# Kernel optimization log

Hardware: AMD Instinct MI355X
Metric: run time of the kernel (lower is better)

## Reference

```python
import jax, jax.numpy as jnp
import numpy as np

EMBED_DIM = 1024
NUM_HEADS = 16
HEAD_DIM = EMBED_DIM // NUM_HEADS


def setup_inputs() -> dict:
    key = jax.random.key(0)
    ks = jax.random.split(key, 9)
    B, S, E = 4, 2048, EMBED_DIM
    # xavier_uniform bound for square [E, E] weights
    bound = float(np.sqrt(6.0 / (E + E)))
    def w(k):
        return jax.random.uniform(k, (E, E), jnp.float32, -bound, bound)
    return {
        "x": jax.random.normal(ks[0], (B, S, E), jnp.float32),
        "Wq": w(ks[1]), "bq": jnp.zeros((E,), jnp.float32),
        "Wk": w(ks[2]), "bk": jnp.zeros((E,), jnp.float32),
        "Wv": w(ks[3]), "bv": jnp.zeros((E,), jnp.float32),
        "Wo": w(ks[4]), "bo": jnp.zeros((E,), jnp.float32),
    }


def reference(x, Wq, bq, Wk, bk, Wv, bv, Wo, bo):
    B, S, E = x.shape
    H, D = NUM_HEADS, HEAD_DIM
    # Linear projections (torch Linear: x @ W.T + b)
    q = (x @ Wq.T + bq).reshape(B, S, H, D)
    k = (x @ Wk.T + bk).reshape(B, S, H, D)
    v = (x @ Wv.T + bv).reshape(B, S, H, D)
    # per-head scaled dot-product attention (vectorized over heads)
    scores = jnp.einsum("bqhd,bkhd->bhqk", q, k) / jnp.sqrt(jnp.float32(D))
    attn = jax.nn.softmax(scores, axis=-1)
    o = jnp.einsum("bhqk,bkhd->bqhd", attn, v).reshape(B, S, E)
    return o @ Wo.T + bo
```

## Files before the change

kernel.cpp:

```cpp
#include <hip/hip_runtime.h>
#include <stdint.h>

typedef unsigned short u16;
typedef short bf16x8 __attribute__((ext_vector_type(8)));
typedef float f32x4 __attribute__((ext_vector_type(4)));
typedef float f32x16 __attribute__((ext_vector_type(16)));

#define B_ 4
#define S_ 2048
#define H_ 16
#define D_ 64
#define E_ 1024
#define M_ (B_ * S_)

static __device__ __forceinline__ u16 f2bf(float f) {
  uint32_t u = __builtin_bit_cast(uint32_t, f);
  u += 0x7fffu + ((u >> 16) & 1u);
  return (u16)(u >> 16);
}
static __device__ __forceinline__ uint32_t pack2bf(float a, float b) {
  return (uint32_t)f2bf(a) | ((uint32_t)f2bf(b) << 16);
}
static __device__ __forceinline__ uint32_t cvt_pk_bf16(float a, float b) {
  uint32_t r;
  asm("v_cvt_pk_bf16_f32 %0, %1, %2" : "=v"(r) : "v"(a), "v"(b));
  return r;
}
static __device__ __forceinline__ void pl32swap(uint32_t& a, uint32_t& b) {
  asm volatile("v_permlane32_swap_b32 %0, %1" : "+v"(a), "+v"(b));
}

static __device__ __forceinline__ void gld_lds16(const void* g, void* l) {
  __builtin_amdgcn_global_load_lds(
      (const __attribute__((address_space(1))) void*)(uintptr_t)g,
      (__attribute__((address_space(3))) void*)(uint32_t)(uintptr_t)l, 16, 0, 0);
}

__global__ __launch_bounds__(256) void cvt_f32_bf16(const float* __restrict__ in,
                                                    u16* __restrict__ out, int n) {
  int i = (blockIdx.x * 256 + threadIdx.x) * 8;
  if (i + 8 > n) return;
  float4 a = *(const float4*)(in + i);
  float4 b = *(const float4*)(in + i + 4);
  struct __align__(16) U8 { u16 h[8]; } u;
  u.h[0] = f2bf(a.x); u.h[1] = f2bf(a.y); u.h[2] = f2bf(a.z); u.h[3] = f2bf(a.w);
  u.h[4] = f2bf(b.x); u.h[5] = f2bf(b.y); u.h[6] = f2bf(b.z); u.h[7] = f2bf(b.w);
  *(U8*)(out + i) = u;
}

__global__ __launch_bounds__(256) void cvt_w4(const float* __restrict__ w0,
                                              const float* __restrict__ w1,
                                              const float* __restrict__ w2,
                                              const float* __restrict__ w3,
                                              u16* __restrict__ out) {
  const int NW_BLK = (E_ * E_) / 2048;
  const int seg = blockIdx.x >> 9;
  const float* src = seg == 0 ? w0 : seg == 1 ? w1 : seg == 2 ? w2 : w3;
  int i = ((blockIdx.x & (NW_BLK - 1)) * 256 + threadIdx.x) * 8;
  float4 a = *(const float4*)(src + i);
  float4 b = *(const float4*)(src + i + 4);
  struct __align__(16) U8 { u16 h[8]; } u;
  u.h[0] = f2bf(a.x); u.h[1] = f2bf(a.y); u.h[2] = f2bf(a.z); u.h[3] = f2bf(a.w);
  u.h[4] = f2bf(b.x); u.h[5] = f2bf(b.y); u.h[6] = f2bf(b.z); u.h[7] = f2bf(b.w);
  *(U8*)(out + (size_t)seg * (E_ * E_) + i) = u;
}

template <int KIND, typename OutT>
static __device__ __forceinline__ void gemm128(const u16* __restrict__ A,
                                               const u16* __restrict__ W,
                                               const float* __restrict__ bias,
                                               OutT* __restrict__ C, int m0, int n0,
                                               float scale, u16* As, u16* Bs) {
  const int tid = threadIdx.x;
  const int wave = tid >> 6, lane = tid & 63;
  const int col16 = lane & 15, quad = lane >> 4;
  const int wm = wave >> 1, wn = wave & 1;

  f32x4 acc[4][4] = {};

  const int r0 = tid >> 3;
  const int sg8 = ((tid & 7) ^ (r0 & 7)) * 8;
  const u16* ga = A + (size_t)(m0 + r0) * E_ + sg8;
  const u16* gb = W + (size_t)(n0 + r0) * E_ + sg8;
  u16* lA = As + wave * 512;
  u16* lB = Bs + wave * 512;

  auto stage = [&](int k0, int buf) {
#pragma unroll
    for (int i = 0; i < 4; i++) {
      gld_lds16(ga + (size_t)(i * 32) * E_ + k0, lA + buf * 8192 + i * 2048);
      gld_lds16(gb + (size_t)(i * 32) * E_ + k0, lB + buf * 8192 + i * 2048);
    }
  };

  stage(0, 0);
  const int NK = E_ / 64;
  for (int kk = 0; kk < NK; kk++) {
    asm volatile("s_waitcnt vmcnt(0)" ::: "memory");
    __builtin_amdgcn_s_barrier();
    if (kk + 1 < NK) stage((kk + 1) * 64, (kk + 1) & 1);

    const u16* AsC = As + (kk & 1) * 8192;
    const u16* BsC = Bs + (kk & 1) * 8192;

    bf16x8 af[4][2], bw[4][2];
#pragma unroll
    for (int mt = 0; mt < 4; mt++)
#pragma unroll
      for (int ks = 0; ks < 2; ks++)
        af[mt][ks] = *(const bf16x8*)&AsC[(wm * 64 + mt * 16 + col16) * 64 +
                                          (((ks * 4 + quad) ^ (col16 & 7)) * 8)];
#pragma unroll
    for (int nt = 0; nt < 4; nt++)
#pragma unroll
      for (int ks = 0; ks < 2; ks++)
        bw[nt][ks] = *(const bf16x8*)&BsC[(wn * 64 + nt * 16 + col16) * 64 +
                                          (((ks * 4 + quad) ^ (col16 & 7)) * 8)];
#pragma unroll
    for (int ks = 0; ks < 2; ks++)
#pragma unroll
      for (int a = 0; a < 4; a++)
#pragma unroll
        for (int b = 0; b < 4; b++) {
          if constexpr (KIND == 2)
            acc[a][b] = __builtin_amdgcn_mfma_f32_16x16x32_bf16(af[a][ks], bw[b][ks], acc[a][b], 0, 0, 0);
          else
            acc[a][b] = __builtin_amdgcn_mfma_f32_16x16x32_bf16(bw[a][ks], af[b][ks], acc[a][b], 0, 0, 0);
        }
  }

  if constexpr (KIND == 2) {
#pragma unroll
    for (int a = 0; a < 4; a++) {
      int t = m0 + wm * 64 + a * 16 + quad * 4;
      int bb = t >> 11, s = t & (S_ - 1);
#pragma unroll
      for (int b = 0; b < 4; b++) {
        int oc = n0 + wn * 64 + b * 16 + col16;
        int h = oc >> 6, d = oc & 63;
        float bv = bias[oc];
        uint32_t lo = pack2bf(acc[a][b][0] + bv, acc[a][b][1] + bv);
        uint32_t hi = pack2bf(acc[a][b][2] + bv, acc[a][b][3] + bv);
        uint2 pk = {lo, hi};
        *(uint2*)&C[(((size_t)(bb * H_ + h) * D_ + d) * S_) + s] = pk;
      }
    }
  } else {
#pragma unroll
    for (int b = 0; b < 4; b++) {
      int row = m0 + wm * 64 + b * 16 + col16;
#pragma unroll
      for (int a = 0; a < 4; a++) {
        int nc = n0 + wn * 64 + a * 16 + quad * 4;
        float4 bv = *(const float4*)&bias[nc];
        float v0 = (acc[a][b][0] + bv.x) * scale;
        float v1 = (acc[a][b][1] + bv.y) * scale;
        float v2 = (acc[a][b][2] + bv.z) * scale;
        float v3 = (acc[a][b][3] + bv.w) * scale;
        if constexpr (KIND == 0) {
          uint2 pk = {pack2bf(v0, v1), pack2bf(v2, v3)};
          *(uint2*)&((u16*)C)[(size_t)row * E_ + nc] = pk;
        } else {
          float4 pk = {v0, v1, v2, v3};
          *(float4*)&((float*)C)[(size_t)row * E_ + nc] = pk;
        }
      }
    }
  }
}

__global__ __launch_bounds__(256) void gemm_qkv(const u16* __restrict__ xb,
                                                const u16* __restrict__ wq, const u16* __restrict__ wk,
                                                const u16* __restrict__ wv,
                                                const float* __restrict__ bq, const float* __restrict__ bk,
                                                const float* __restrict__ bv,
                                                u16* __restrict__ Qb, u16* __restrict__ Kb,
                                                u16* __restrict__ Vtb) {
  __shared__ __align__(16) u16 As[2][128 * 64];
  __shared__ __align__(16) u16 Bs[2][128 * 64];
  const int mat = blockIdx.x >> 3;
  const int n0 = (blockIdx.x & 7) * 128;
  const int m0 = blockIdx.y * 128;
  if (mat == 0)
    gemm128<0, u16>(xb, wq, bq, Qb, m0, n0, 0.125f * 1.44269504f, &As[0][0], &Bs[0][0]);
  else if (mat == 1)
    gemm128<0, u16>(xb, wk, bk, Kb, m0, n0, 1.0f, &As[0][0], &Bs[0][0]);
  else
    gemm128<2, u16>(xb, wv, bv, Vtb, m0, n0, 1.0f, &As[0][0], &Bs[0][0]);
}

__global__ __launch_bounds__(256) void gemm_out(const u16* __restrict__ Ob,
                                                const u16* __restrict__ wob,
                                                const float* __restrict__ bo,
                                                float* __restrict__ out) {
  __shared__ __align__(16) u16 As[2][128 * 64];
  __shared__ __align__(16) u16 Bs[2][128 * 64];
  gemm128<1, float>(Ob, wob, bo, out, blockIdx.y * 128, blockIdx.x * 128, 1.0f,
                    &As[0][0], &Bs[0][0]);
}

__global__ __launch_bounds__(512) void flash_attn(const u16* __restrict__ Q,
                                                  const u16* __restrict__ K,
                                                  const u16* __restrict__ Vt,
                                                  u16* __restrict__ O) {
  __shared__ __align__(16) u16 Ks[2][2][64 * 64];
  __shared__ __align__(16) u16 Vs[2][2][64 * 64];
  const int bid = blockIdx.x;
  const int qt = bid & 7, h = (bid >> 3) & 15, b = bid >> 7;
  const int tid = threadIdx.x;
  const int wave = tid >> 6, lane = tid & 63;
  const int l31 = lane & 31, hi = lane >> 5;
  const int sw7 = l31 & 7;

  const int srow = tid >> 3;
  const int sgrp = (tid & 7) ^ (srow & 7);
  const u16* Kbase = K + ((size_t)(b * S_) * H_ + h) * D_;
  const u16* Vbase = Vt + ((size_t)(b * H_ + h) * D_) * S_;

  auto stage = [&](int r, int buf) {
#pragma unroll
    for (int sub = 0; sub < 2; sub++) {
      gld_lds16(Kbase + (size_t)(r * 128 + sub * 64 + srow) * (H_ * D_) + sgrp * 8,
                &Ks[buf][sub][wave * 512]);
      gld_lds16(Vbase + (size_t)srow * S_ + r * 128 + sub * 64 + sgrp * 8,
                &Vs[buf][sub][wave * 512]);
    }
  };

  stage(0, 0);

  const int qrow = qt * 256 + wave * 32;
  bf16x8 qf[4];
  const u16* qp = Q + ((size_t)(b * S_ + qrow + l31) * H_ + h) * D_ + hi * 8;
#pragma unroll
  for (int t = 0; t < 4; t++) qf[t] = *(const bf16x8*)(qp + t * 16);

  f32x16 o_acc[2] = {};
  float l_sum = 0.f;

  const int NR = S_ / 128;
  for (int r = 0; r < NR; r++) {
    asm volatile("s_waitcnt vmcnt(0)" ::: "memory");
    __builtin_amdgcn_s_barrier();
    if (r + 1 < NR) stage(r + 1, (r + 1) & 1);
    const u16* KsC = &Ks[r & 1][0][0];
    const u16* VsC = &Vs[r & 1][0][0];

#pragma unroll
    for (int kblk = 0; kblk < 4; kblk++) {
      const u16* Ksub = KsC + (kblk >> 1) * 4096;
      const u16* Vsub = VsC + (kblk >> 1) * 4096;
      const int krow = (kblk & 1) * 32 + l31;
      f32x16 sacc = {};
      __builtin_amdgcn_s_setprio(1);
#pragma unroll
      for (int t = 0; t < 4; t++) {
        bf16x8 kf = *(const bf16x8*)&Ksub[krow * 64 + (((2 * t + hi) ^ sw7) * 8)];
        sacc = __builtin_amdgcn_mfma_f32_32x32x16_bf16(kf, qf[t], sacc, 0, 0, 0);
      }
      __builtin_amdgcn_s_setprio(0);

      float p[16];
#pragma unroll
      for (int e = 0; e < 16; e++) p[e] = __builtin_amdgcn_exp2f(sacc[e]);
      float s0 = (p[0] + p[1]) + (p[2] + p[3]);
      float s1 = (p[4] + p[5]) + (p[6] + p[7]);
      float s2 = (p[8] + p[9]) + (p[10] + p[11]);
      float s3 = (p[12] + p[13]) + (p[14] + p[15]);
      l_sum += (s0 + s1) + (s2 + s3);
      uint32_t W[8];
#pragma unroll
      for (int i = 0; i < 8; i++) W[i] = cvt_pk_bf16(p[2 * i], p[2 * i + 1]);

#pragma unroll
      for (int kf2 = 0; kf2 < 2; kf2++) {
        uint32_t w0 = W[kf2 * 4 + 0], w1 = W[kf2 * 4 + 1];
        uint32_t w2 = W[kf2 * 4 + 2], w3 = W[kf2 * 4 + 3];
        pl32swap(w0, w2);
        pl32swap(w1, w3);
        union { uint32_t w[4]; bf16x8 v; } u;
        u.w[0] = w0; u.w[1] = w1; u.w[2] = w2; u.w[3] = w3;
        const bf16x8 pa = u.v;
        const int kfs = (kblk & 1) * 2 + kf2;
        __builtin_amdgcn_s_setprio(1);
#pragma unroll
        for (int n = 0; n < 2; n++) {
          const int dr = n * 32 + l31;
          bf16x8 vf = *(const bf16x8*)&Vsub[dr * 64 + (((2 * kfs + hi) ^ sw7) * 8)];
          o_acc[n] = __builtin_amdgcn_mfma_f32_32x32x16_bf16(pa, vf, o_acc[n], 0, 0, 0);
        }
        __builtin_amdgcn_s_setprio(0);
      }
    }
  }

  float l_tot = l_sum + __shfl_xor(l_sum, 32);
  float inv = 1.f / l_tot;

#pragma unroll
  for (int r = 0; r < 16; r++) {
    const int ql = (r & 3) + 8 * (r >> 2) + 4 * hi;
    const float iq = __shfl(inv, ql);
    u16* op = O + ((size_t)(b * S_ + qrow + ql) * H_ + h) * D_ + l31;
#pragma unroll
    for (int n = 0; n < 2; n++) op[n * 32] = f2bf(o_acc[n][r] * iq);
  }
}

extern "C" void kernel_launch(void* const* d_in, const int* in_sizes, int n_in,
                              void* d_out, int out_size, void* d_ws, size_t ws_size,
                              hipStream_t stream) {
  (void)in_sizes; (void)n_in; (void)out_size; (void)ws_size;
  const float* x  = (const float*)d_in[0];
  const float* Wq = (const float*)d_in[1];
  const float* bq = (const float*)d_in[2];
  const float* Wk = (const float*)d_in[3];
  const float* bk = (const float*)d_in[4];
  const float* Wv = (const float*)d_in[5];
  const float* bv = (const float*)d_in[6];
  const float* Wo = (const float*)d_in[7];
  const float* bo = (const float*)d_in[8];
  float* out = (float*)d_out;

  const size_t NX = (size_t)M_ * E_;
  const size_t NW = (size_t)E_ * E_;
  u16* xb  = (u16*)d_ws;
  u16* wqb = xb + NX;
  u16* wkb = wqb + NW;
  u16* wvb = wkb + NW;
  u16* wob = wvb + NW;
  u16* Qb  = wob + NW;
  u16* Kb  = Qb + NX;
  u16* Vtb = Kb + NX;
  u16* Ob  = Vtb + NX;

  cvt_f32_bf16<<<NX / 2048, 256, 0, stream>>>(x, xb, (int)NX);
  cvt_w4<<<4 * (NW / 2048), 256, 0, stream>>>(Wq, Wk, Wv, Wo, wqb);

  gemm_qkv<<<dim3(24, 64), 256, 0, stream>>>(xb, wqb, wkb, wvb, bq, bk, bv, Qb, Kb, Vtb);
  flash_attn<<<B_ * H_ * (S_ / 256), 512, 0, stream>>>(Qb, Kb, Vtb, Ob);
  gemm_out<<<dim3(8, 64), 256, 0, stream>>>(Ob, wob, bo, out);
}
```

Measured before the change: 275.0 us.

## Process two query groups per wave in flash attention with 256-thread blocks

Each wave now handles 64 query rows as two 32-row groups, so every K and V fragment read from LDS feeds two MFMAs instead of one. Blocks shrink from 8 to 4 waves, and the staging loop issues twice as many loads per thread to fill the same K/V tiles. This halves LDS read traffic per MFMA. In exchange it doubles the accumulator and Q registers per wave and leaves fewer waves per block to hide latency, with launch bounds set to allow two blocks per CU.

```diff
diff --git a/kernel.cpp b/kernel.cpp
--- a/kernel.cpp
+++ b/kernel.cpp
@@ -199,10 +199,10 @@
                     &As[0][0], &Bs[0][0]);
 }
 
-__global__ __launch_bounds__(512) void flash_attn(const u16* __restrict__ Q,
-                                                  const u16* __restrict__ K,
-                                                  const u16* __restrict__ Vt,
-                                                  u16* __restrict__ O) {
+__global__ __launch_bounds__(256, 2) void flash_attn(const u16* __restrict__ Q,
+                                                     const u16* __restrict__ K,
+                                                     const u16* __restrict__ Vt,
+                                                     u16* __restrict__ O) {
   __shared__ __align__(16) u16 Ks[2][2][64 * 64];
   __shared__ __align__(16) u16 Vs[2][2][64 * 64];
   const int bid = blockIdx.x;
@@ -219,24 +219,29 @@
 
   auto stage = [&](int r, int buf) {
 #pragma unroll
-    for (int sub = 0; sub < 2; sub++) {
-      gld_lds16(Kbase + (size_t)(r * 128 + sub * 64 + srow) * (H_ * D_) + sgrp * 8,
-                &Ks[buf][sub][wave * 512]);
-      gld_lds16(Vbase + (size_t)srow * S_ + r * 128 + sub * 64 + sgrp * 8,
-                &Vs[buf][sub][wave * 512]);
-    }
+    for (int sub = 0; sub < 2; sub++)
+#pragma unroll
+      for (int half = 0; half < 2; half++) {
+        gld_lds16(Kbase + (size_t)(r * 128 + sub * 64 + half * 32 + srow) * (H_ * D_) + sgrp * 8,
+                  &Ks[buf][sub][half * 2048 + wave * 512]);
+        gld_lds16(Vbase + (size_t)(half * 32 + srow) * S_ + r * 128 + sub * 64 + sgrp * 8,
+                  &Vs[buf][sub][half * 2048 + wave * 512]);
+      }
   };
 
   stage(0, 0);
 
-  const int qrow = qt * 256 + wave * 32;
-  bf16x8 qf[4];
-  const u16* qp = Q + ((size_t)(b * S_ + qrow + l31) * H_ + h) * D_ + hi * 8;
-#pragma unroll
-  for (int t = 0; t < 4; t++) qf[t] = *(const bf16x8*)(qp + t * 16);
-
-  f32x16 o_acc[2] = {};
-  float l_sum = 0.f;
+  const int qrow = qt * 256 + wave * 64;
+  bf16x8 qf[2][4];
+#pragma unroll
+  for (int qg = 0; qg < 2; qg++) {
+    const u16* qp = Q + ((size_t)(b * S_ + qrow + qg * 32 + l31) * H_ + h) * D_ + hi * 8;
+#pragma unroll
+    for (int t = 0; t < 4; t++) qf[qg][t] = *(const bf16x8*)(qp + t * 16);
+  }
+
+  f32x16 o_acc[2][2] = {};
+  float l_sum[2] = {0.f, 0.f};
 
   const int NR = S_ / 128;
   for (int r = 0; r < NR; r++) {
@@ -251,59 +256,75 @@
       const u16* Ksub = KsC + (kblk >> 1) * 4096;
       const u16* Vsub = VsC + (kblk >> 1) * 4096;
       const int krow = (kblk & 1) * 32 + l31;
-      f32x16 sacc = {};
+      bf16x8 kf[4];
+#pragma unroll
+      for (int t = 0; t < 4; t++)
+        kf[t] = *(const bf16x8*)&Ksub[krow * 64 + (((2 * t + hi) ^ sw7) * 8)];
+      f32x16 sacc[2];
+      sacc[0] = (f32x16)0.f; sacc[1] = (f32x16)0.f;
       __builtin_amdgcn_s_setprio(1);
 #pragma unroll
       for (int t = 0; t < 4; t++) {
-        bf16x8 kf = *(const bf16x8*)&Ksub[krow * 64 + (((2 * t + hi) ^ sw7) * 8)];
-        sacc = __builtin_amdgcn_mfma_f32_32x32x16_bf16(kf, qf[t], sacc, 0, 0, 0);
+        sacc[0] = __builtin_amdgcn_mfma_f32_32x32x16_bf16(kf[t], qf[0][t], sacc[0], 0, 0, 0);
+        sacc[1] = __builtin_amdgcn_mfma_f32_32x32x16_bf16(kf[t], qf[1][t], sacc[1], 0, 0, 0);
       }
       __builtin_amdgcn_s_setprio(0);
 
-      float p[16];
-#pragma unroll
-      for (int e = 0; e < 16; e++) p[e] = __builtin_amdgcn_exp2f(sacc[e]);
-      float s0 = (p[0] + p[1]) + (p[2] + p[3]);
-      float s1 = (p[4] + p[5]) + (p[6] + p[7]);
-      float s2 = (p[8] + p[9]) + (p[10] + p[11]);
-      float s3 = (p[12] + p[13]) + (p[14] + p[15]);
-      l_sum += (s0 + s1) + (s2 + s3);
-      uint32_t W[8];
-#pragma unroll
-      for (int i = 0; i < 8; i++) W[i] = cvt_pk_bf16(p[2 * i], p[2 * i + 1]);
+      uint32_t W[2][8];
+#pragma unroll
+      for (int qg = 0; qg < 2; qg++) {
+        float p[16];
+#pragma unroll
+        for (int e = 0; e < 16; e++) p[e] = __builtin_amdgcn_exp2f(sacc[qg][e]);
+        float s0 = (p[0] + p[1]) + (p[2] + p[3]);
+        float s1 = (p[4] + p[5]) + (p[6] + p[7]);
+        float s2 = (p[8] + p[9]) + (p[10] + p[11]);
+        float s3 = (p[12] + p[13]) + (p[14] + p[15]);
+        l_sum[qg] += (s0 + s1) + (s2 + s3);
+#pragma unroll
+        for (int i = 0; i < 8; i++) W[qg][i] = cvt_pk_bf16(p[2 * i], p[2 * i + 1]);
+      }
 
 #pragma unroll
       for (int kf2 = 0; kf2 < 2; kf2++) {
-        uint32_t w0 = W[kf2 * 4 + 0], w1 = W[kf2 * 4 + 1];
-        uint32_t w2 = W[kf2 * 4 + 2], w3 = W[kf2 * 4 + 3];
-        pl32swap(w0, w2);
-        pl32swap(w1, w3);
-        union { uint32_t w[4]; bf16x8 v; } u;
-        u.w[0] = w0; u.w[1] = w1; u.w[2] = w2; u.w[3] = w3;
-        const bf16x8 pa = u.v;
+        bf16x8 pa[2];
+#pragma unroll
+        for (int qg = 0; qg < 2; qg++) {
+          uint32_t w0 = W[qg][kf2 * 4 + 0], w1 = W[qg][kf2 * 4 + 1];
+          uint32_t w2 = W[qg][kf2 * 4 + 2], w3 = W[qg][kf2 * 4 + 3];
+          pl32swap(w0, w2);
+          pl32swap(w1, w3);
+          union { uint32_t w[4]; bf16x8 v; } u;
+          u.w[0] = w0; u.w[1] = w1; u.w[2] = w2; u.w[3] = w3;
+          pa[qg] = u.v;
+        }
         const int kfs = (kblk & 1) * 2 + kf2;
         __builtin_amdgcn_s_setprio(1);
 #pragma unroll
         for (int n = 0; n < 2; n++) {
           const int dr = n * 32 + l31;
           bf16x8 vf = *(const bf16x8*)&Vsub[dr * 64 + (((2 * kfs + hi) ^ sw7) * 8)];
-          o_acc[n] = __builtin_amdgcn_mfma_f32_32x32x16_bf16(pa, vf, o_acc[n], 0, 0, 0);
+          o_acc[0][n] = __builtin_amdgcn_mfma_f32_32x32x16_bf16(pa[0], vf, o_acc[0][n], 0, 0, 0);
+          o_acc[1][n] = __builtin_amdgcn_mfma_f32_32x32x16_bf16(pa[1], vf, o_acc[1][n], 0, 0, 0);
         }
         __builtin_amdgcn_s_setprio(0);
       }
     }
   }
 
-  float l_tot = l_sum + __shfl_xor(l_sum, 32);
-  float inv = 1.f / l_tot;
-
-#pragma unroll
-  for (int r = 0; r < 16; r++) {
-    const int ql = (r & 3) + 8 * (r >> 2) + 4 * hi;
-    const float iq = __shfl(inv, ql);
-    u16* op = O + ((size_t)(b * S_ + qrow + ql) * H_ + h) * D_ + l31;
-#pragma unroll
-    for (int n = 0; n < 2; n++) op[n * 32] = f2bf(o_acc[n][r] * iq);
+#pragma unroll
+  for (int qg = 0; qg < 2; qg++) {
+    float l_tot = l_sum[qg] + __shfl_xor(l_sum[qg], 32);
+    float inv = 1.f / l_tot;
+
+#pragma unroll
+    for (int r = 0; r < 16; r++) {
+      const int ql = (r & 3) + 8 * (r >> 2) + 4 * hi;
+      const float iq = __shfl(inv, ql);
+      u16* op = O + ((size_t)(b * S_ + qrow + qg * 32 + ql) * H_ + h) * D_ + l31;
+#pragma unroll
+      for (int n = 0; n < 2; n++) op[n * 32] = f2bf(o_acc[qg][n][r] * iq);
+    }
   }
 }
 
@@ -338,6 +359,6 @@
   cvt_w4<<<4 * (NW / 2048), 256, 0, stream>>>(Wq, Wk, Wv, Wo, wqb);
 
   gemm_qkv<<<dim3(24, 64), 256, 0, stream>>>(xb, wqb, wkb, wvb, bq, bk, bv, Qb, Kb, Vtb);
-  flash_attn<<<B_ * H_ * (S_ / 256), 512, 0, stream>>>(Qb, Kb, Vtb, Ob);
+  flash_attn<<<B_ * H_ * (S_ / 256), 256, 0, stream>>>(Qb, Kb, Vtb, Ob);
   gemm_out<<<dim3(8, 64), 256, 0, stream>>>(Ob, wob, bo, out);
 }
```

Result: no change. 278.6 us (+1.3%).

## Pre-swizzle V into MFMA fragment order and load directly to registers

Applied to the files above, without the earlier changes.

The V projection epilogue now writes V in a per-head layout that matches the MFMA B-operand fragment order, so the attention kernel can load V fragments from global memory straight into registers. This removes V from shared memory. K staging moves to a triple-buffered 64-row ring with a prefetch distance of two, waited on with vmcnt(1), and launch bounds request 4 blocks per SM. The aim is to cut LDS traffic and capacity so occupancy can rise, at the cost of uncached-through-LDS global loads for V on every tile, more register pressure from holding eight V fragments, and more frequent barriers.

```diff
diff --git a/kernel.cpp b/kernel.cpp
--- a/kernel.cpp
+++ b/kernel.cpp
@@ -134,15 +134,20 @@
     for (int a = 0; a < 4; a++) {
       int t = m0 + wm * 64 + a * 16 + quad * 4;
       int bb = t >> 11, s = t & (S_ - 1);
+      int kb = s >> 6, w = s & 63;
+      int kfs = w >> 4, hi2 = (w >> 3) & 1, j0 = w & 7;
 #pragma unroll
       for (int b = 0; b < 4; b++) {
         int oc = n0 + wn * 64 + b * 16 + col16;
         int h = oc >> 6, d = oc & 63;
+        int nn = d >> 5, ld = d & 31;
         float bv = bias[oc];
         uint32_t lo = pack2bf(acc[a][b][0] + bv, acc[a][b][1] + bv);
         uint32_t hi = pack2bf(acc[a][b][2] + bv, acc[a][b][3] + bv);
         uint2 pk = {lo, hi};
-        *(uint2*)&C[(((size_t)(bb * H_ + h) * D_ + d) * S_) + s] = pk;
+        size_t off = (size_t)(bb * H_ + h) * (S_ * D_) + kb * 4096 +
+                     (nn * 4 + kfs) * 512 + ld * 16 + hi2 * 8 + j0;
+        *(uint2*)&C[off] = pk;
       }
     }
   } else {
@@ -175,7 +180,7 @@
                                                 const float* __restrict__ bq, const float* __restrict__ bk,
                                                 const float* __restrict__ bv,
                                                 u16* __restrict__ Qb, u16* __restrict__ Kb,
-                                                u16* __restrict__ Vtb) {
+                                                u16* __restrict__ V2b) {
   __shared__ __align__(16) u16 As[2][128 * 64];
   __shared__ __align__(16) u16 Bs[2][128 * 64];
   const int mat = blockIdx.x >> 3;
@@ -186,7 +191,7 @@
   else if (mat == 1)
     gemm128<0, u16>(xb, wk, bk, Kb, m0, n0, 1.0f, &As[0][0], &Bs[0][0]);
   else
-    gemm128<2, u16>(xb, wv, bv, Vtb, m0, n0, 1.0f, &As[0][0], &Bs[0][0]);
+    gemm128<2, u16>(xb, wv, bv, V2b, m0, n0, 1.0f, &As[0][0], &Bs[0][0]);
 }
 
 __global__ __launch_bounds__(256) void gemm_out(const u16* __restrict__ Ob,
@@ -199,12 +204,11 @@
                     &As[0][0], &Bs[0][0]);
 }
 
-__global__ __launch_bounds__(512) void flash_attn(const u16* __restrict__ Q,
-                                                  const u16* __restrict__ K,
-                                                  const u16* __restrict__ Vt,
-                                                  u16* __restrict__ O) {
-  __shared__ __align__(16) u16 Ks[2][2][64 * 64];
-  __shared__ __align__(16) u16 Vs[2][2][64 * 64];
+__global__ __launch_bounds__(512, 4) void flash_attn(const u16* __restrict__ Q,
+                                                     const u16* __restrict__ K,
+                                                     const u16* __restrict__ V2,
+                                                     u16* __restrict__ O) {
+  __shared__ __align__(16) u16 Ks[3][64 * 64];
   const int bid = blockIdx.x;
   const int qt = bid & 7, h = (bid >> 3) & 15, b = bid >> 7;
   const int tid = threadIdx.x;
@@ -215,19 +219,15 @@
   const int srow = tid >> 3;
   const int sgrp = (tid & 7) ^ (srow & 7);
   const u16* Kbase = K + ((size_t)(b * S_) * H_ + h) * D_;
-  const u16* Vbase = Vt + ((size_t)(b * H_ + h) * D_) * S_;
-
-  auto stage = [&](int r, int buf) {
-#pragma unroll
-    for (int sub = 0; sub < 2; sub++) {
-      gld_lds16(Kbase + (size_t)(r * 128 + sub * 64 + srow) * (H_ * D_) + sgrp * 8,
-                &Ks[buf][sub][wave * 512]);
-      gld_lds16(Vbase + (size_t)srow * S_ + r * 128 + sub * 64 + sgrp * 8,
-                &Vs[buf][sub][wave * 512]);
-    }
+  const u16* vp = V2 + (size_t)(b * H_ + h) * (S_ * D_) + l31 * 16 + hi * 8;
+
+  auto stageK = [&](int kb, int buf) {
+    gld_lds16(Kbase + (size_t)(kb * 64 + srow) * (H_ * D_) + sgrp * 8,
+              &Ks[buf][wave * 512]);
   };
 
-  stage(0, 0);
+  stageK(0, 0);
+  stageK(1, 1);
 
   const int qrow = qt * 256 + wave * 32;
   bf16x8 qf[4];
@@ -238,24 +238,33 @@
   f32x16 o_acc[2] = {};
   float l_sum = 0.f;
 
-  const int NR = S_ / 128;
-  for (int r = 0; r < NR; r++) {
-    asm volatile("s_waitcnt vmcnt(0)" ::: "memory");
+  const int NT = S_ / 64;
+  int cur = 0;
+  for (int kb = 0; kb < NT; kb++) {
+    asm volatile("s_waitcnt vmcnt(1)" ::: "memory");
     __builtin_amdgcn_s_barrier();
-    if (r + 1 < NR) stage(r + 1, (r + 1) & 1);
-    const u16* KsC = &Ks[r & 1][0][0];
-    const u16* VsC = &Vs[r & 1][0][0];
-
-#pragma unroll
-    for (int kblk = 0; kblk < 4; kblk++) {
-      const u16* Ksub = KsC + (kblk >> 1) * 4096;
-      const u16* Vsub = VsC + (kblk >> 1) * 4096;
-      const int krow = (kblk & 1) * 32 + l31;
+
+    bf16x8 vf[2][4];
+#pragma unroll
+    for (int n = 0; n < 2; n++)
+#pragma unroll
+      for (int kfs = 0; kfs < 4; kfs++)
+        vf[n][kfs] = *(const bf16x8*)(vp + (size_t)kb * 4096 + (n * 4 + kfs) * 512);
+
+    if (kb + 2 < NT) {
+      int nb = cur + 2; if (nb >= 3) nb -= 3;
+      stageK(kb + 2, nb);
+    }
+    const u16* KsC = Ks[cur];
+
+#pragma unroll
+    for (int kblk = 0; kblk < 2; kblk++) {
+      const int krow = kblk * 32 + l31;
       f32x16 sacc = {};
       __builtin_amdgcn_s_setprio(1);
 #pragma unroll
       for (int t = 0; t < 4; t++) {
-        bf16x8 kf = *(const bf16x8*)&Ksub[krow * 64 + (((2 * t + hi) ^ sw7) * 8)];
+        bf16x8 kf = *(const bf16x8*)&KsC[krow * 64 + (((2 * t + hi) ^ sw7) * 8)];
         sacc = __builtin_amdgcn_mfma_f32_32x32x16_bf16(kf, qf[t], sacc, 0, 0, 0);
       }
       __builtin_amdgcn_s_setprio(0);
@@ -281,17 +290,14 @@
         union { uint32_t w[4]; bf16x8 v; } u;
         u.w[0] = w0; u.w[1] = w1; u.w[2] = w2; u.w[3] = w3;
         const bf16x8 pa = u.v;
-        const int kfs = (kblk & 1) * 2 + kf2;
+        const int kfs = kblk * 2 + kf2;
         __builtin_amdgcn_s_setprio(1);
-#pragma unroll
-        for (int n = 0; n < 2; n++) {
-          const int dr = n * 32 + l31;
-          bf16x8 vf = *(const bf16x8*)&Vsub[dr * 64 + (((2 * kfs + hi) ^ sw7) * 8)];
-          o_acc[n] = __builtin_amdgcn_mfma_f32_32x32x16_bf16(pa, vf, o_acc[n], 0, 0, 0);
-        }
+        o_acc[0] = __builtin_amdgcn_mfma_f32_32x32x16_bf16(pa, vf[0][kfs], o_acc[0], 0, 0, 0);
+        o_acc[1] = __builtin_amdgcn_mfma_f32_32x32x16_bf16(pa, vf[1][kfs], o_acc[1], 0, 0, 0);
         __builtin_amdgcn_s_setprio(0);
       }
     }
+    cur = (cur + 1 == 3) ? 0 : cur + 1;
   }
 
   float l_tot = l_sum + __shfl_xor(l_sum, 32);
@@ -331,13 +337,13 @@
   u16* wob = wvb + NW;
   u16* Qb  = wob + NW;
   u16* Kb  = Qb + NX;
-  u16* Vtb = Kb + NX;
-  u16* Ob  = Vtb + NX;
+  u16* V2b = Kb + NX;
+  u16* Ob  = V2b + NX;
 
   cvt_f32_bf16<<<NX / 2048, 256, 0, stream>>>(x, xb, (int)NX);
   cvt_w4<<<4 * (NW / 2048), 256, 0, stream>>>(Wq, Wk, Wv, Wo, wqb);
 
-  gemm_qkv<<<dim3(24, 64), 256, 0, stream>>>(xb, wqb, wkb, wvb, bq, bk, bv, Qb, Kb, Vtb);
-  flash_attn<<<B_ * H_ * (S_ / 256), 512, 0, stream>>>(Qb, Kb, Vtb, Ob);
+  gemm_qkv<<<dim3(24, 64), 256, 0, stream>>>(xb, wqb, wkb, wvb, bq, bk, bv, Qb, Kb, V2b);
+  flash_attn<<<B_ * H_ * (S_ / 256), 512, 0, stream>>>(Qb, Kb, V2b, Ob);
   gemm_out<<<dim3(8, 64), 256, 0, stream>>>(Ob, wob, bo, out);
 }
```

New measurement: 338.2 us. 23.0% more time.
